# Kernel optimization log

Measured on AMD Instinct MI355X. Metric: run time of the kernel, lower is better.

Reference implementation:

```python
import jax, jax.numpy as jnp
import numpy as np

N = 64000      # total nodes in batched graph (16 graphs x 4000)
E = 1024000    # total edges (avg degree 16)
D = 512        # input/output feature dim
KTOT = 2048    # total assign dim (128 clusters per graph)
B = 16         # batch size (number of graphs)


def setup_inputs() -> dict:
    key = jax.random.key(0)
    ks = jax.random.split(key, 5)
    feat = jax.random.normal(ks[0], (N, D), jnp.float32)
    W_feat = jax.random.normal(ks[1], (D, D), jnp.float32) / np.float32(np.sqrt(D))
    b_feat = jnp.zeros((D,), jnp.float32)
    W_pool = jax.random.normal(ks[2], (D, KTOT), jnp.float32) / np.float32(np.sqrt(D))
    b_pool = jnp.zeros((KTOT,), jnp.float32)
    src = jax.random.randint(ks[3], (E,), 0, N, dtype=jnp.int32)
    dst = jax.random.randint(ks[4], (E,), 0, N, dtype=jnp.int32)
    return {"feat": feat, "W_feat": W_feat, "b_feat": b_feat,
            "W_pool": W_pool, "b_pool": b_pool,
            "src": src, "dst": dst, "batch_size": B}


def _gin(x, src, dst, W, b):
    """GIN layer with mean aggregator: relu(W @ (x + mean_neighbors(x)) + b)."""
    n = x.shape[0]
    agg = jax.ops.segment_sum(x[src], dst, num_segments=n)              # [N, d_in]
    deg = jax.ops.segment_sum(jnp.ones((src.shape[0],), x.dtype), dst, num_segments=n)
    agg = agg / jnp.maximum(deg, 1.0)[:, None]
    return jax.nn.relu((x + agg) @ W + b)


def reference(feat, W_feat, b_feat, W_pool, b_pool, src, dst, batch_size):
    n = feat.shape[0]
    ktot = W_pool.shape[1]
    n_per = n // batch_size      # equal-sized graphs (batch_num_nodes)
    k_per = ktot // batch_size   # clusters per graph

    h_feat = _gin(feat, src, dst, W_feat, b_feat)    # [N, D]
    assign = _gin(feat, src, dst, W_pool, b_pool)    # [N, KTOT]

    # block_diag mask: node of graph b may only assign to columns of graph b
    gid_node = jnp.arange(n) // n_per                # [N]
    gid_col = jnp.arange(ktot) // k_per              # [KTOT]
    mask = (gid_node[:, None] == gid_col[None, :]).astype(assign.dtype)

    # allennlp masked_softmax(memory_efficient=False):
    # softmax(x * mask) * mask, renormalized with +1e-13
    s = jax.nn.softmax(assign * mask, axis=-1) * mask
    s = s / (s.sum(axis=-1, keepdims=True) + 1e-13)  # [N, KTOT]

    h = s.T @ h_feat                                 # [KTOT, D]
    # sparse adj @ S via edge-list scatter: (A S)[i] = sum_{(i,j) in E} S[j]
    adj_s = jax.ops.segment_sum(s[dst], src, num_segments=n)  # [N, KTOT]
    adj_new = s.T @ adj_s                            # [KTOT, KTOT]
    return adj_new, h
```

## Files before the change

### kernel.cpp

```cpp
#include <hip/hip_runtime.h>
#include <math.h>

constexpr int N  = 64000;
constexpr int E  = 1024000;
constexpr int D  = 512;
constexpr int KT = 2048;
constexpr int B  = 16;
constexpr int NP = 4000;
constexpr int KP = 128;
constexpr int NR = N / 256;
constexpr int EPB = 2048;
constexpr int NPB = E / EPB;
constexpr int RSTRIDE = 4608;
constexpr int BSTRIDE = 4608;

typedef __attribute__((ext_vector_type(4))) float f32x4;
typedef __attribute__((ext_vector_type(2))) float f32x2;
typedef __attribute__((ext_vector_type(8))) short bf16x8;
typedef __attribute__((ext_vector_type(8))) unsigned short u16x8;

__device__ __forceinline__ unsigned short f2bf(float f) {
    unsigned u = __builtin_bit_cast(unsigned, f);
    return (unsigned short)((u + 0x7FFFu + ((u >> 16) & 1u)) >> 16);
}
__device__ __forceinline__ float bf2f(unsigned short h) {
    unsigned u = (unsigned)h << 16;
    return __builtin_bit_cast(float, u);
}

__device__ __forceinline__ unsigned char f2fp8_sw(float f) {
    unsigned u = __builtin_bit_cast(unsigned, f);
    unsigned s = u >> 31;
    float a = fabsf(f);
    if (a > 448.f) a = 448.f;
    unsigned code;
    if (a < 0.015625f) {
        code = (unsigned)rintf(a * 512.0f);
    } else {
        unsigned au = __builtin_bit_cast(unsigned, a);
        unsigned mant = au & 0x7FFFFFu;
        unsigned rnd = 0x7FFFFu + ((mant >> 20) & 1u);
        unsigned r2 = au + rnd;
        int e = (int)(r2 >> 23) - 127;
        unsigned m3 = (r2 >> 20) & 7u;
        if (e > 8) { e = 8; m3 = 7; }
        code = (unsigned)((e + 7) << 3) | m3;
    }
    return (unsigned char)(code | (s << 7));
}
__device__ __forceinline__ float fp82f_sw(unsigned b) {
    unsigned s = b >> 7, e = (b >> 3) & 15u, m = b & 7u;
    float vn = __builtin_bit_cast(float, ((e + 120u) << 23) | (m << 20));
    float vs = (float)(int)m * 0x1p-9f;
    float v = e ? vn : vs;
    return s ? -v : v;
}

__device__ __forceinline__ unsigned char f2fp8(float f) {
#if __has_builtin(__builtin_amdgcn_cvt_pk_fp8_f32)
    int w = __builtin_amdgcn_cvt_pk_fp8_f32(f, 0.f, 0, false);
    return (unsigned char)(w & 0xFF);
#else
    return f2fp8_sw(f);
#endif
}

__device__ __forceinline__ unsigned pack4_fp8(float f0, float f1, float f2, float f3) {
#if __has_builtin(__builtin_amdgcn_cvt_pk_fp8_f32)
    int w = __builtin_amdgcn_cvt_pk_fp8_f32(f0, f1, 0, false);
    w = __builtin_amdgcn_cvt_pk_fp8_f32(f2, f3, w, true);
    return (unsigned)w;
#else
    return (unsigned)f2fp8_sw(f0) | ((unsigned)f2fp8_sw(f1) << 8) |
           ((unsigned)f2fp8_sw(f2) << 16) | ((unsigned)f2fp8_sw(f3) << 24);
#endif
}

__device__ __forceinline__ void acc8_fp8(float* a, uint2 w) {
#if __has_builtin(__builtin_amdgcn_cvt_pk_f32_fp8)
    f32x2 p0 = __builtin_amdgcn_cvt_pk_f32_fp8((int)w.x, false);
    f32x2 p1 = __builtin_amdgcn_cvt_pk_f32_fp8((int)w.x, true);
    f32x2 p2 = __builtin_amdgcn_cvt_pk_f32_fp8((int)w.y, false);
    f32x2 p3 = __builtin_amdgcn_cvt_pk_f32_fp8((int)w.y, true);
    a[0] += p0.x; a[1] += p0.y; a[2] += p1.x; a[3] += p1.y;
    a[4] += p2.x; a[5] += p2.y; a[6] += p3.x; a[7] += p3.y;
#else
    #pragma unroll
    for (int q = 0; q < 4; ++q) a[q] += fp82f_sw((w.x >> (8 * q)) & 255u);
    #pragma unroll
    for (int q = 0; q < 4; ++q) a[4 + q] += fp82f_sw((w.y >> (8 * q)) & 255u);
#endif
}

typedef const __attribute__((address_space(1))) unsigned int* gas_u32p;
typedef __attribute__((address_space(3))) unsigned int* las_u32p;
__device__ __forceinline__ void glds16(const unsigned short* g, unsigned short* l) {
    __builtin_amdgcn_global_load_lds((gas_u32p)(const void*)g, (las_u32p)(void*)l, 16, 0, 0);
}

__device__ __forceinline__ int block_incl_scan(int v, int* ws) {
    int t = threadIdx.x, lane = t & 63, w = t >> 6;
    int x = v;
    #pragma unroll
    for (int off = 1; off < 64; off <<= 1) {
        int y = __shfl_up(x, off);
        if (lane >= off) x += y;
    }
    if (lane == 63) ws[w] = x;
    __syncthreads();
    if (t < 4) {
        int s = ws[t];
        #pragma unroll
        for (int off = 1; off < 4; off <<= 1) {
            int y = __shfl_up(s, off);
            if (t >= off) s += y;
        }
        ws[t] = s;
    }
    __syncthreads();
    return x + (w > 0 ? ws[w - 1] : 0);
}

__global__ __launch_bounds__(256) void k_cvt(const float* __restrict__ in,
                                             unsigned short* __restrict__ outb,
                                             unsigned char* __restrict__ out8,
                                             long long n) {
    long long i = ((long long)blockIdx.x * 256 + threadIdx.x) * 8;
    if (i >= n) return;
    f32x4 a = *(const f32x4*)&in[i];
    f32x4 b = *(const f32x4*)&in[i + 4];
    u16x8 o;
    o[0] = f2bf(a.x); o[1] = f2bf(a.y); o[2] = f2bf(a.z); o[3] = f2bf(a.w);
    o[4] = f2bf(b.x); o[5] = f2bf(b.y); o[6] = f2bf(b.z); o[7] = f2bf(b.w);
    *(u16x8*)&outb[i] = o;
    uint2 w;
    w.x = pack4_fp8(a.x, a.y, a.z, a.w);
    w.y = pack4_fp8(b.x, b.y, b.z, b.w);
    *(uint2*)&out8[i] = w;
}

__global__ void k_zrow(unsigned short* __restrict__ fb,
                       unsigned short* __restrict__ scb,
                       unsigned short* __restrict__ hfb,
                       unsigned char* __restrict__ f8b,
                       unsigned char* __restrict__ sc8) {
    int t = threadIdx.x;
    const u16x8 Z = {0, 0, 0, 0, 0, 0, 0, 0};
    if (t < 64)        *(u16x8*)&fb[(size_t)N * D + t * 8] = Z;
    else if (t < 80)   *(u16x8*)&scb[(size_t)N * KP + (t - 64) * 8] = Z;
    else if (t < 144)  *(u16x8*)&hfb[(size_t)N * D + (t - 80) * 8] = Z;
    else if (t < 176)  *(u16x8*)&f8b[(size_t)N * D + (size_t)(t - 144) * 16] = Z;
    else if (t < 184)  *(u16x8*)&sc8[(size_t)N * KP + (size_t)(t - 176) * 16] = Z;
}

__global__ __launch_bounds__(256) void k_transpose(const float* __restrict__ in,
                                                   unsigned short* __restrict__ out,
                                                   int R, int C) {
    __shared__ float tile[32][33];
    int bx = blockIdx.x * 32, by = blockIdx.y * 32;
    int tx = threadIdx.x & 31, ty = threadIdx.x >> 5;
    #pragma unroll
    for (int i = 0; i < 32; i += 8)
        if (by + ty + i < R && bx + tx < C)
            tile[ty + i][tx] = in[(size_t)(by + ty + i) * C + bx + tx];
    __syncthreads();
    #pragma unroll
    for (int i = 0; i < 32; i += 8)
        if (bx + ty + i < C && by + tx < R)
            out[(size_t)(bx + ty + i) * R + by + tx] = f2bf(tile[tx][ty + i]);
}

__global__ void k_init(int* __restrict__ rcur, int* __restrict__ bcur) {
    int t = threadIdx.x;
    if (t < NR) rcur[t] = t * RSTRIDE;
    bcur[t] = t * BSTRIDE;
}

__global__ __launch_bounds__(256) void k_split(const int* __restrict__ src,
                                               const int* __restrict__ dst,
                                               int* __restrict__ rcur, int2* __restrict__ out1,
                                               int* __restrict__ bcur, int2* __restrict__ out2) {
    __shared__ int2 stg[EPB];
    __shared__ int h[256], lstart[256], gbase[256];
    __shared__ int ws[4];
    int t = threadIdx.x;
    int e0 = blockIdx.x * EPB;
    int sv[8], dv[8], bin[8], rank[8];
    #pragma unroll
    for (int i = 0; i < 8; ++i) {
        int e = e0 + t + i * 256;
        sv[i] = src[e]; dv[i] = dst[e];
    }
    h[t] = 0;
    __syncthreads();
    #pragma unroll
    for (int i = 0; i < 8; ++i) {
        bin[i] = dv[i] >> 8;
        rank[i] = atomicAdd(&h[bin[i]], 1);
    }
    __syncthreads();
    {
        int v = h[t];
        int incl = block_incl_scan(v, ws);
        lstart[t] = incl - v;
        gbase[t] = v ? atomicAdd(&rcur[t], v) : 0;
    }
    __syncthreads();
    #pragma unroll
    for (int i = 0; i < 8; ++i)
        stg[lstart[bin[i]] + rank[i]] = int2{sv[i], dv[i]};
    __syncthreads();
    for (int i = t; i < EPB; i += 256) {
        int2 e = stg[i];
        int b = e.y >> 8;
        out1[gbase[b] + i - lstart[b]] = e;
    }
    __syncthreads();
    h[t] = 0;
    __syncthreads();
    #pragma unroll
    for (int i = 0; i < 8; ++i) {
        bin[i] = (sv[i] / NP) * B + dv[i] / NP;
        rank[i] = atomicAdd(&h[bin[i]], 1);
    }
    __syncthreads();
    {
        int v = h[t];
        int incl = block_incl_scan(v, ws);
        lstart[t] = incl - v;
        gbase[t] = v ? atomicAdd(&bcur[t], v) : 0;
    }
    __syncthreads();
    #pragma unroll
    for (int i = 0; i < 8; ++i)
        stg[lstart[bin[i]] + rank[i]] = int2{sv[i], dv[i]};
    __syncthreads();
    for (int i = t; i < EPB; i += 256) {
        int2 e = stg[i];
        int b = (e.x / NP) * B + e.y / NP;
        out2[gbase[b] + i - lstart[b]] = e;
    }
}

__global__ __launch_bounds__(256) void k_part2(const int2* __restrict__ pairs,
                                               const int* __restrict__ rcur,
                                               int* __restrict__ rowstart,
                                               int* __restrict__ degv,
                                               int* __restrict__ csr) {
    __shared__ int h[256];
    __shared__ int ws[4];
    int t = threadIdx.x;
    int r = blockIdx.x;
    int p0 = r * RSTRIDE, p1 = rcur[r];
    h[t] = 0;
    __syncthreads();
    for (int p = p0 + t; p < p1; p += 256)
        atomicAdd(&h[pairs[p].y & 255], 1);
    __syncthreads();
    int v = h[t];
    int incl = block_incl_scan(v, ws);
    int start = p0 + incl - v;
    __syncthreads();
    h[t] = start;
    rowstart[r * 256 + t] = start;
    degv[r * 256 + t] = v;
    __syncthreads();
    for (int p = p0 + t; p < p1; p += 256) {
        int2 e = pairs[p];
        int pos = atomicAdd(&h[e.y & 255], 1);
        csr[pos] = e.x;
    }
}

__global__ __launch_bounds__(256) void k_agg(const unsigned short* __restrict__ fb,
                                             const unsigned char* __restrict__ f8,
                                             const int* __restrict__ rowstart,
                                             const int* __restrict__ degv,
                                             const int* __restrict__ csr,
                                             unsigned short* __restrict__ xb) {
    int w = threadIdx.x >> 6, lane = threadIdx.x & 63;
    int node = blockIdx.x * 4 + w;
    int r0 = rowstart[node], dg = degv[node], r1 = r0 + dg;
    u16x8 self = *(const u16x8*)&fb[(size_t)node * D + lane * 8];
    float a[8] = {};
    for (int base = r0; base < r1; base += 64) {
        int ii = base + lane;
        int idx = N;
        if (ii < r1) idx = csr[ii];
        int cnt = r1 - base; if (cnt > 64) cnt = 64;
        int batches = (cnt + 7) & ~7;
        for (int j = 0; j < batches; j += 8) {
            int s0 = __shfl(idx, j + 0), s1 = __shfl(idx, j + 1);
            int s2 = __shfl(idx, j + 2), s3 = __shfl(idx, j + 3);
            int s4 = __shfl(idx, j + 4), s5 = __shfl(idx, j + 5);
            int s6 = __shfl(idx, j + 6), s7 = __shfl(idx, j + 7);
            uint2 g0 = *(const uint2*)&f8[(size_t)s0 * D + lane * 8];
            uint2 g1 = *(const uint2*)&f8[(size_t)s1 * D + lane * 8];
            uint2 g2 = *(const uint2*)&f8[(size_t)s2 * D + lane * 8];
            uint2 g3 = *(const uint2*)&f8[(size_t)s3 * D + lane * 8];
            uint2 g4 = *(const uint2*)&f8[(size_t)s4 * D + lane * 8];
            uint2 g5 = *(const uint2*)&f8[(size_t)s5 * D + lane * 8];
            uint2 g6 = *(const uint2*)&f8[(size_t)s6 * D + lane * 8];
            uint2 g7 = *(const uint2*)&f8[(size_t)s7 * D + lane * 8];
            acc8_fp8(a, g0); acc8_fp8(a, g1); acc8_fp8(a, g2); acc8_fp8(a, g3);
            acc8_fp8(a, g4); acc8_fp8(a, g5); acc8_fp8(a, g6); acc8_fp8(a, g7);
        }
    }
    float inv = 1.0f / fmaxf((float)dg, 1.0f);
    u16x8 o;
    #pragma unroll
    for (int q = 0; q < 8; ++q) o[q] = f2bf(bf2f(self[q]) + a[q] * inv);
    *(u16x8*)&xb[(size_t)node * D + lane * 8] = o;
}

__global__ __launch_bounds__(256) void k_gemm_feat(const unsigned short* __restrict__ Xb,
                                                   const unsigned short* __restrict__ Wt,
                                                   const float* __restrict__ bias,
                                                   unsigned short* __restrict__ Hf) {
    __shared__ unsigned short As[128 * 64];
    __shared__ unsigned short Bs[128 * 64];
    int t = threadIdx.x, wid = t >> 6, lane = t & 63;
    int wm = wid >> 1, wn = wid & 1;
    int row0 = blockIdx.x * 128, col0 = blockIdx.y * 128;
    int r8 = lane >> 3, ch = (lane & 7) ^ r8;
    f32x4 acc[4][4] = {};
    for (int k0 = 0; k0 < D; k0 += 64) {
        #pragma unroll
        for (int i = 0; i < 4; ++i) {
            int rr = wid * 32 + i * 8;
            glds16(Xb + (size_t)(row0 + rr + r8) * D + k0 + ch * 8, As + rr * 64);
            glds16(Wt + (size_t)(col0 + rr + r8) * D + k0 + ch * 8, Bs + rr * 64);
        }
        __syncthreads();
        #pragma unroll
        for (int ks = 0; ks < 2; ++ks) {
            bf16x8 af[4], bfr[4];
            #pragma unroll
            for (int f = 0; f < 4; ++f) {
                int ra = wm * 64 + f * 16 + (lane & 15);
                af[f] = *(const bf16x8*)&As[ra * 64 + (((ks * 4 + (lane >> 4)) ^ (ra & 7)) << 3)];
                int rb = wn * 64 + f * 16 + (lane & 15);
                bfr[f] = *(const bf16x8*)&Bs[rb * 64 + (((ks * 4 + (lane >> 4)) ^ (rb & 7)) << 3)];
            }
            #pragma unroll
            for (int m = 0; m < 4; ++m)
                #pragma unroll
                for (int n = 0; n < 4; ++n)
                    acc[m][n] = __builtin_amdgcn_mfma_f32_16x16x32_bf16(af[m], bfr[n], acc[m][n], 0, 0, 0);
        }
        __syncthreads();
    }
    float bv[4];
    #pragma unroll
    for (int n = 0; n < 4; ++n) bv[n] = bias[col0 + wn * 64 + n * 16 + (lane & 15)];
    #pragma unroll
    for (int m = 0; m < 4; ++m)
        #pragma unroll
        for (int r = 0; r < 4; ++r) {
            int row = row0 + wm * 64 + m * 16 + (lane >> 4) * 4 + r;
            #pragma unroll
            for (int n = 0; n < 4; ++n) {
                int col = col0 + wn * 64 + n * 16 + (lane & 15);
                float v = fmaxf(acc[m][n][r] + bv[n], 0.f);
                Hf[(size_t)row * D + col] = f2bf(v);
            }
        }
}

__global__ __launch_bounds__(256) void k_gemm_pool(const unsigned short* __restrict__ Xb,
                                                   const unsigned short* __restrict__ Wpt,
                                                   const float* __restrict__ bp,
                                                   unsigned short* __restrict__ sc,
                                                   unsigned char* __restrict__ sc8) {
    __shared__ unsigned short As[128 * 64];
    __shared__ unsigned short Bs[128 * 64];
    int t = threadIdx.x, wid = t >> 6, lane = t & 63;
    int bm = blockIdx.x;
    int g  = blockIdx.y;
    int row0 = g * NP + bm * 128;
    int nrows = NP - bm * 128; if (nrows > 128) nrows = 128;
    int col0 = g * KP;
    int r8 = lane >> 3, ch = (lane & 7) ^ r8;
    f32x4 acc[2][8] = {};
    for (int k0 = 0; k0 < D; k0 += 64) {
        #pragma unroll
        for (int i = 0; i < 4; ++i) {
            int rr = wid * 32 + i * 8;
            glds16(Xb + (size_t)(row0 + rr + r8) * D + k0 + ch * 8, As + rr * 64);
            glds16(Wpt + (size_t)(col0 + rr + r8) * D + k0 + ch * 8, Bs + rr * 64);
        }
        __syncthreads();
        #pragma unroll
        for (int ks = 0; ks < 2; ++ks) {
            bf16x8 af[2], bfr[8];
            #pragma unroll
            for (int m = 0; m < 2; ++m) {
                int ra = wid * 32 + m * 16 + (lane & 15);
                af[m] = *(const bf16x8*)&As[ra * 64 + (((ks * 4 + (lane >> 4)) ^ (ra & 7)) << 3)];
            }
            #pragma unroll
            for (int n = 0; n < 8; ++n) {
                int rb = n * 16 + (lane & 15);
                bfr[n] = *(const bf16x8*)&Bs[rb * 64 + (((ks * 4 + (lane >> 4)) ^ (rb & 7)) << 3)];
            }
            #pragma unroll
            for (int m = 0; m < 2; ++m)
                #pragma unroll
                for (int n = 0; n < 8; ++n)
                    acc[m][n] = __builtin_amdgcn_mfma_f32_16x16x32_bf16(af[m], bfr[n], acc[m][n], 0, 0, 0);
        }
        __syncthreads();
    }
    float bv[8];
    #pragma unroll
    for (int n = 0; n < 8; ++n) bv[n] = bp[col0 + n * 16 + (lane & 15)];
    #pragma unroll
    for (int m = 0; m < 2; ++m)
        #pragma unroll
        for (int r = 0; r < 4; ++r) {
            float v[8];
            #pragma unroll
            for (int n = 0; n < 8; ++n) v[n] = fmaxf(acc[m][n][r] + bv[n], 0.f);
            float mx = v[0];
            #pragma unroll
            for (int n = 1; n < 8; ++n) mx = fmaxf(mx, v[n]);
            #pragma unroll
            for (int off = 1; off < 16; off <<= 1) mx = fmaxf(mx, __shfl_xor(mx, off));
            float ssum = 0.f;
            #pragma unroll
            for (int n = 0; n < 8; ++n) { v[n] = __expf(v[n] - mx); ssum += v[n]; }
            #pragma unroll
            for (int off = 1; off < 16; off <<= 1) ssum += __shfl_xor(ssum, off);
            float inv = 1.0f / ssum;
            int rowl = wid * 32 + m * 16 + (lane >> 4) * 4 + r;
            if (rowl < nrows) {
                #pragma unroll
                for (int n = 0; n < 8; ++n) {
                    float sv = v[n] * inv;
                    int col = n * 16 + (lane & 15);
                    sc[(size_t)(row0 + rowl) * KP + col] = f2bf(sv);
                    sc8[(size_t)(row0 + rowl) * KP + col] = f2fp8(sv * 16.0f);
                }
            }
        }
}

constexpr int VBASE = 4128;
constexpr int VB8   = 4128;
constexpr int ADJ_SPLIT = 4;
constexpr int KZ_H = 16;

__device__ __forceinline__ void uv_write(unsigned short* arr, int c0, int es,
                                         const u16x8& l0, const u16x8& l1,
                                         const u16x8& l2, const u16x8& l3) {
    #pragma unroll
    for (int q = 0; q < 8; ++q) {
        int r0 = c0 + q, r1 = c0 + 8 + q, r2 = c0 + 16 + q, r3 = c0 + 24 + q;
        arr[r0 * 32 + (es ^ (((r0 >> 1) & 3) << 3))] = l0[q];
        arr[r1 * 32 + (es ^ (((r1 >> 1) & 3) << 3))] = l1[q];
        arr[r2 * 32 + (es ^ (((r2 >> 1) & 3) << 3))] = l2[q];
        arr[r3 * 32 + (es ^ (((r3 >> 1) & 3) << 3))] = l3[q];
    }
}

__device__ __forceinline__ void row_load(const unsigned short* row,
                                         u16x8& l0, u16x8& l1, u16x8& l2, u16x8& l3) {
    l0 = *(const u16x8*)(row);
    l1 = *(const u16x8*)(row + 8);
    l2 = *(const u16x8*)(row + 16);
    l3 = *(const u16x8*)(row + 24);
}

__device__ __forceinline__ bf16x8 uv_read(const unsigned short* UV, int base,
                                          int row, int chunk) {
    int c = chunk ^ ((row >> 1) & 3);
    return *(const bf16x8*)&UV[base + row * 32 + c * 8];
}

__device__ __forceinline__ void h_body(unsigned short* UV,
                                       const unsigned short* __restrict__ sc,
                                       const unsigned short* __restrict__ hf,
                                       float* __restrict__ outH,
                                       int g, int nt, int kz) {
    int t = threadIdx.x, wid = t >> 6, lane = t & 63;
    int n0 = nt * 128;
    int i0 = g * NP + kz * (NP / KZ_H), i1 = i0 + NP / KZ_H;
    int c0 = wid * 32;
    int es = lane & 31, op = lane >> 5;
    unsigned short* arr = &UV[op * VBASE];
    f32x4 acc[2][8] = {};

    const unsigned short* baseptr = op ? (hf + n0 + c0) : (sc + c0);
    int rstride = op ? D : KP;
    auto mkrow = [&](int tbase) -> const unsigned short* {
        int nd = tbase + es;
        nd = nd < i1 ? nd : N;
        return baseptr + (size_t)nd * rstride;
    };

    u16x8 a0, a1, a2, a3, b0, b1, b2, b3;
    row_load(mkrow(i0), a0, a1, a2, a3);
    row_load(mkrow(i0 + 32), b0, b1, b2, b3);

    int ntile = (i1 - i0 + 31) >> 5;
    for (int tt = 0; tt < ntile; tt += 2) {
        __syncthreads();
        uv_write(arr, c0, es, a0, a1, a2, a3);
        __syncthreads();
        row_load(mkrow(i0 + (tt + 2) * 32), a0, a1, a2, a3);
        {
            bf16x8 af[2], bfr[8];
            #pragma unroll
            for (int m = 0; m < 2; ++m)
                af[m] = uv_read(UV, 0, wid * 32 + m * 16 + (lane & 15), lane >> 4);
            #pragma unroll
            for (int n = 0; n < 8; ++n)
                bfr[n] = uv_read(UV, VBASE, n * 16 + (lane & 15), lane >> 4);
            #pragma unroll
            for (int m = 0; m < 2; ++m)
                #pragma unroll
                for (int n = 0; n < 8; ++n)
                    acc[m][n] = __builtin_amdgcn_mfma_f32_16x16x32_bf16(af[m], bfr[n], acc[m][n], 0, 0, 0);
        }
        __syncthreads();
        uv_write(arr, c0, es, b0, b1, b2, b3);
        __syncthreads();
        row_load(mkrow(i0 + (tt + 3) * 32), b0, b1, b2, b3);
        {
            bf16x8 af[2], bfr[8];
            #pragma unroll
            for (int m = 0; m < 2; ++m)
                af[m] = uv_read(UV, 0, wid * 32 + m * 16 + (lane & 15), lane >> 4);
            #pragma unroll
            for (int n = 0; n < 8; ++n)
                bfr[n] = uv_read(UV, VBASE, n * 16 + (lane & 15), lane >> 4);
            #pragma unroll
            for (int m = 0; m < 2; ++m)
                #pragma unroll
                for (int n = 0; n < 8; ++n)
                    acc[m][n] = __builtin_amdgcn_mfma_f32_16x16x32_bf16(af[m], bfr[n], acc[m][n], 0, 0, 0);
        }
    }
    #pragma unroll
    for (int m = 0; m < 2; ++m)
        #pragma unroll
        for (int r = 0; r < 4; ++r) {
            int row = g * KP + wid * 32 + m * 16 + (lane >> 4) * 4 + r;
            #pragma unroll
            for (int n = 0; n < 8; ++n) {
                int col = n0 + n * 16 + (lane & 15);
                atomicAdd(&outH[(size_t)row * D + col], acc[m][n][r]);
            }
        }
}

__device__ __forceinline__ void uv_write8(unsigned char* arr, int c0, int es,
                                          const uint4& lo, const uint4& hi) {
    const unsigned* wsrc = (const unsigned*)&lo;
    const unsigned* wsrc2 = (const unsigned*)&hi;
    int eb = es & 7, ec = es >> 3;
    #pragma unroll
    for (int q = 0; q < 8; ++q) {
        unsigned w0 = wsrc[q >> 1], w1 = wsrc2[q >> 1];
        #pragma unroll
        for (int hb = 0; hb < 2; ++hb) {
            int qi = q * 2 + hb;
            {
                int row = c0 + qi;
                unsigned byte = (wsrc[qi >> 2] >> ((qi & 3) * 8)) & 255u;
                arr[row * 32 + (((ec ^ ((row >> 2) & 3)) << 3) | eb)] = (unsigned char)byte;
            }
            {
                int row = c0 + 16 + qi;
                unsigned byte = (wsrc2[qi >> 2] >> ((qi & 3) * 8)) & 255u;
                arr[row * 32 + (((ec ^ ((row >> 2) & 3)) << 3) | eb)] = (unsigned char)byte;
            }
        }
    }
}

__device__ __forceinline__ long long uv_read8(const unsigned char* UV8, int base,
                                              int row, int chunk) {
    int c = chunk ^ ((row >> 2) & 3);
    return *(const long long*)&UV8[base + row * 32 + c * 8];
}

__device__ __forceinline__ void adj_body(unsigned char* UV8,
                                         const unsigned char* __restrict__ sc8,
                                         const int2* __restrict__ bpairs,
                                         const int* __restrict__ bcur,
                                         float* __restrict__ outA,
                                         int g1, int g2, int part) {
    int t = threadIdx.x, wid = t >> 6, lane = t & 63;
    int b = g1 * B + g2;
    int e0 = b * BSTRIDE, e1 = bcur[b], cnt = e1 - e0;
    int s0 = e0 + (int)((long long)cnt * part / ADJ_SPLIT);
    int s1 = e0 + (int)((long long)cnt * (part + 1) / ADJ_SPLIT);
    int c0 = wid * 32;
    int es = lane & 31, op = lane >> 5;
    unsigned char* arr = &UV8[op * VB8];
    f32x4 acc[2][8] = {};

    auto mkrow = [&](int tbase) -> const unsigned char* {
        int idx = tbase + es;
        bool v = idx < s1;
        int2 e = bpairs[v ? idx : s0];
        int node = v ? (op ? e.y : e.x) : N;
        return sc8 + (size_t)node * KP + c0;
    };

    uint4 alo, ahi, blo, bhi;
    { const unsigned char* r = mkrow(s0);      alo = *(const uint4*)r; ahi = *(const uint4*)(r + 16); }
    { const unsigned char* r = mkrow(s0 + 32); blo = *(const uint4*)r; bhi = *(const uint4*)(r + 16); }

    int ntile = (s1 - s0 + 31) >> 5;
    for (int tt = 0; tt < ntile; tt += 2) {
        __syncthreads();
        uv_write8(arr, c0, es, alo, ahi);
        __syncthreads();
        { const unsigned char* r = mkrow(s0 + (tt + 2) * 32); alo = *(const uint4*)r; ahi = *(const uint4*)(r + 16); }
        {
            long long af[2], bfr[8];
            #pragma unroll
            for (int m = 0; m < 2; ++m)
                af[m] = uv_read8(UV8, 0, wid * 32 + m * 16 + (lane & 15), lane >> 4);
            #pragma unroll
            for (int n = 0; n < 8; ++n)
                bfr[n] = uv_read8(UV8, VB8, n * 16 + (lane & 15), lane >> 4);
            #pragma unroll
            for (int m = 0; m < 2; ++m)
                #pragma unroll
                for (int n = 0; n < 8; ++n)
                    acc[m][n] = __builtin_amdgcn_mfma_f32_16x16x32_fp8_fp8(af[m], bfr[n], acc[m][n], 0, 0, 0);
        }
        __syncthreads();
        uv_write8(arr, c0, es, blo, bhi);
        __syncthreads();
        { const unsigned char* r = mkrow(s0 + (tt + 3) * 32); blo = *(const uint4*)r; bhi = *(const uint4*)(r + 16); }
        {
            long long af[2], bfr[8];
            #pragma unroll
            for (int m = 0; m < 2; ++m)
                af[m] = uv_read8(UV8, 0, wid * 32 + m * 16 + (lane & 15), lane >> 4);
            #pragma unroll
            for (int n = 0; n < 8; ++n)
                bfr[n] = uv_read8(UV8, VB8, n * 16 + (lane & 15), lane >> 4);
            #pragma unroll
            for (int m = 0; m < 2; ++m)
                #pragma unroll
                for (int n = 0; n < 8; ++n)
                    acc[m][n] = __builtin_amdgcn_mfma_f32_16x16x32_fp8_fp8(af[m], bfr[n], acc[m][n], 0, 0, 0);
        }
    }
    const float DS = 1.0f / 256.0f;
    #pragma unroll
    for (int m = 0; m < 2; ++m)
        #pragma unroll
        for (int r = 0; r < 4; ++r) {
            int row = g1 * KP + wid * 32 + m * 16 + (lane >> 4) * 4 + r;
            #pragma unroll
            for (int n = 0; n < 8; ++n) {
                int col = g2 * KP + n * 16 + (lane & 15);
                atomicAdd(&outA[(size_t)row * KT + col], acc[m][n][r] * DS);
            }
        }
}

__global__ __launch_bounds__(256) void k_ha(const unsigned short* __restrict__ sc,
                                            const unsigned char* __restrict__ sc8,
                                            const unsigned short* __restrict__ hf,
                                            const int2* __restrict__ bpairs,
                                            const int* __restrict__ bcur,
                                            float* __restrict__ outH,
                                            float* __restrict__ outA) {
    __shared__ __align__(16) unsigned short UV[8224];
    int lin = blockIdx.x;
    int role = (lin >> 8) & 1;
    int base = (lin >> 9) * 256 + (lin & 255);
    if (role == 0) {
        int xcd = base & 7, idx = base >> 3;
        int g1 = 2 * xcd + (idx & 1);
        int g2 = (idx >> 1) & 15;
        int part = (idx >> 5) & 3;
        adj_body((unsigned char*)UV, sc8, bpairs, bcur, outA, g1, g2, part);
    } else {
        int g = base & 15, nt = (base >> 4) & 3, kz = base >> 6;
        h_body(UV, sc, hf, outH, g, nt, kz);
    }
}

extern "C" void kernel_launch(void* const* d_in, const int* in_sizes, int n_in,
                              void* d_out, int out_size, void* d_ws, size_t ws_size,
                              hipStream_t stream) {
    const float* feat   = (const float*)d_in[0];
    const float* W_feat = (const float*)d_in[1];
    const float* b_feat = (const float*)d_in[2];
    const float* W_pool = (const float*)d_in[3];
    const float* b_pool = (const float*)d_in[4];
    const int*   src    = (const int*)d_in[5];
    const int*   dst    = (const int*)d_in[6];

    char* w = (char*)d_ws;
    unsigned short* fb  = (unsigned short*)w; w += (size_t)(N + 1) * D * 2;
    unsigned char*  f8b = (unsigned char*)w;  w += (size_t)(N + 1) * D;
    unsigned short* xb  = (unsigned short*)w; w += (size_t)N * D * 2;
    unsigned short* hfb = (unsigned short*)w; w += (size_t)(N + 1) * D * 2;
    unsigned short* scb = (unsigned short*)w; w += (size_t)(N + 1) * KP * 2;
    unsigned char*  sc8 = (unsigned char*)w;  w += (size_t)(N + 1) * KP;
    unsigned short* Wt  = (unsigned short*)w; w += (size_t)D * D * 2;
    unsigned short* Wpt = (unsigned short*)w; w += (size_t)KT * D * 2;
    int2* pairs1  = (int2*)w; w += (size_t)NR * RSTRIDE * 8;
    int2* bpairs  = (int2*)w; w += (size_t)256 * BSTRIDE * 8;
    int*  csr     = (int*)w;  w += ((size_t)NR * RSTRIDE + 64) * 4;
    int*  rowstart= (int*)w;  w += (size_t)N * 4;
    int*  degv    = (int*)w;  w += (size_t)N * 4;
    int*  rcur    = (int*)w;  w += NR * 4;
    int*  bcur    = (int*)w;  w += 256 * 4;

    hipMemsetAsync(d_out, 0, (size_t)out_size * sizeof(float), stream);

    k_cvt<<<(int)(((long long)N * D) / (8 * 256)), 256, 0, stream>>>(feat, fb, f8b, (long long)N * D);
    k_zrow<<<1, 256, 0, stream>>>(fb, scb, hfb, f8b, sc8);
    dim3 gt1(D / 32, D / 32);
    k_transpose<<<gt1, 256, 0, stream>>>(W_feat, Wt, D, D);
    dim3 gt2(KT / 32, D / 32);
    k_transpose<<<gt2, 256, 0, stream>>>(W_pool, Wpt, D, KT);

    k_init<<<1, 256, 0, stream>>>(rcur, bcur);
    k_split<<<NPB, 256, 0, stream>>>(src, dst, rcur, pairs1, bcur, bpairs);
    k_part2<<<NR, 256, 0, stream>>>(pairs1, rcur, rowstart, degv, csr);

    k_agg<<<N / 4, 256, 0, stream>>>(fb, f8b, rowstart, degv, csr, xb);
    dim3 gf(N / 128, D / 128);
    k_gemm_feat<<<gf, 256, 0, stream>>>(xb, Wt, b_feat, hfb);
    dim3 gp(32, B);
    k_gemm_pool<<<gp, 256, 0, stream>>>(xb, Wpt, b_pool, scb, sc8);

    k_ha<<<2048, 256, 0, stream>>>(scb, sc8, hfb, bpairs, bcur,
                                   (float*)d_out + (size_t)KT * KT, (float*)d_out);
}
```

Before: 407.8 us.

## Split edge bucketing into two passes and double adjacency work split

```diff
diff --git a/kernel.cpp b/kernel.cpp
--- a/kernel.cpp
+++ b/kernel.cpp
@@ -176,10 +176,9 @@
     bcur[t] = t * BSTRIDE;
 }
 
-__global__ __launch_bounds__(256) void k_split(const int* __restrict__ src,
-                                               const int* __restrict__ dst,
-                                               int* __restrict__ rcur, int2* __restrict__ out1,
-                                               int* __restrict__ bcur, int2* __restrict__ out2) {
+__global__ __launch_bounds__(256) void k_splitA(const int* __restrict__ src,
+                                                const int* __restrict__ dst,
+                                                int* __restrict__ rcur, int2* __restrict__ out1) {
     __shared__ int2 stg[EPB];
     __shared__ int h[256], lstart[256], gbase[256];
     __shared__ int ws[4];
@@ -215,13 +214,32 @@
         int b = e.y >> 8;
         out1[gbase[b] + i - lstart[b]] = e;
     }
-    __syncthreads();
+}
+
+__global__ __launch_bounds__(256) void k_splitB(const int2* __restrict__ pairs,
+                                                const int* __restrict__ rcur,
+                                                int* __restrict__ bcur, int2* __restrict__ out2) {
+    __shared__ int2 stg[RSTRIDE / 2];
+    __shared__ int h[256], lstart[256], gbase[256];
+    __shared__ int ws[4];
+    int t = threadIdx.x;
+    int r = blockIdx.x >> 1, half = blockIdx.x & 1;
+    int p0 = r * RSTRIDE, p1 = rcur[r], len = p1 - p0;
+    int s0 = p0 + (len * half) / 2;
+    int s1 = p0 + (len * (half + 1)) / 2;
+    int cnt = s1 - s0;
+    int sv[9], dv[9], bin[9], rank[9];
     h[t] = 0;
     __syncthreads();
     #pragma unroll
-    for (int i = 0; i < 8; ++i) {
-        bin[i] = (sv[i] / NP) * B + dv[i] / NP;
-        rank[i] = atomicAdd(&h[bin[i]], 1);
+    for (int i = 0; i < 9; ++i) {
+        int p = s0 + t + i * 256;
+        if (p < s1) {
+            int2 e = pairs[p];
+            sv[i] = e.x; dv[i] = e.y;
+            bin[i] = (e.x / NP) * B + e.y / NP;
+            rank[i] = atomicAdd(&h[bin[i]], 1);
+        }
     }
     __syncthreads();
     {
@@ -232,10 +250,13 @@
     }
     __syncthreads();
     #pragma unroll
-    for (int i = 0; i < 8; ++i)
-        stg[lstart[bin[i]] + rank[i]] = int2{sv[i], dv[i]};
-    __syncthreads();
-    for (int i = t; i < EPB; i += 256) {
+    for (int i = 0; i < 9; ++i) {
+        int p = s0 + t + i * 256;
+        if (p < s1)
+            stg[lstart[bin[i]] + rank[i]] = int2{sv[i], dv[i]};
+    }
+    __syncthreads();
+    for (int i = t; i < cnt; i += 256) {
         int2 e = stg[i];
         int b = (e.x / NP) * B + e.y / NP;
         out2[gbase[b] + i - lstart[b]] = e;
@@ -447,7 +468,7 @@
 
 constexpr int VBASE = 4128;
 constexpr int VB8   = 4128;
-constexpr int ADJ_SPLIT = 4;
+constexpr int ADJ_SPLIT = 8;
 constexpr int KZ_H = 16;
 
 __device__ __forceinline__ void uv_write(unsigned short* arr, int c0, int es,
@@ -560,21 +581,16 @@
     const unsigned* wsrc2 = (const unsigned*)&hi;
     int eb = es & 7, ec = es >> 3;
     #pragma unroll
-    for (int q = 0; q < 8; ++q) {
-        unsigned w0 = wsrc[q >> 1], w1 = wsrc2[q >> 1];
-        #pragma unroll
-        for (int hb = 0; hb < 2; ++hb) {
-            int qi = q * 2 + hb;
-            {
-                int row = c0 + qi;
-                unsigned byte = (wsrc[qi >> 2] >> ((qi & 3) * 8)) & 255u;
-                arr[row * 32 + (((ec ^ ((row >> 2) & 3)) << 3) | eb)] = (unsigned char)byte;
-            }
-            {
-                int row = c0 + 16 + qi;
-                unsigned byte = (wsrc2[qi >> 2] >> ((qi & 3) * 8)) & 255u;
-                arr[row * 32 + (((ec ^ ((row >> 2) & 3)) << 3) | eb)] = (unsigned char)byte;
-            }
+    for (int qi = 0; qi < 16; ++qi) {
+        {
+            int row = c0 + qi;
+            unsigned byte = (wsrc[qi >> 2] >> ((qi & 3) * 8)) & 255u;
+            arr[row * 32 + (((ec ^ ((row >> 2) & 3)) << 3) | eb)] = (unsigned char)byte;
+        }
+        {
+            int row = c0 + 16 + qi;
+            unsigned byte = (wsrc2[qi >> 2] >> ((qi & 3) * 8)) & 255u;
+            arr[row * 32 + (((ec ^ ((row >> 2) & 3)) << 3) | eb)] = (unsigned char)byte;
         }
     }
 }
@@ -675,17 +691,19 @@
                                             float* __restrict__ outA) {
     __shared__ __align__(16) unsigned short UV[8224];
     int lin = blockIdx.x;
-    int role = (lin >> 8) & 1;
-    int base = (lin >> 9) * 256 + (lin & 255);
-    if (role == 0) {
+    int k = lin >> 8, rem = lin & 255;
+    if (k % 3 == 2) {
+        int hbase = (k / 3) * 256 + rem;
+        int g = hbase & 15, nt = (hbase >> 4) & 3, kz = hbase >> 6;
+        h_body(UV, sc, hf, outH, g, nt, kz);
+    } else {
+        int adjIdx = k - (k + 1) / 3;
+        int base = adjIdx * 256 + rem;
         int xcd = base & 7, idx = base >> 3;
         int g1 = 2 * xcd + (idx & 1);
         int g2 = (idx >> 1) & 15;
-        int part = (idx >> 5) & 3;
+        int part = (idx >> 5) & 7;
         adj_body((unsigned char*)UV, sc8, bpairs, bcur, outA, g1, g2, part);
-    } else {
-        int g = base & 15, nt = (base >> 4) & 3, kz = base >> 6;
-        h_body(UV, sc, hf, outH, g, nt, kz);
     }
 }
 
@@ -727,7 +745,8 @@
     k_transpose<<<gt2, 256, 0, stream>>>(W_pool, Wpt, D, KT);
 
     k_init<<<1, 256, 0, stream>>>(rcur, bcur);
-    k_split<<<NPB, 256, 0, stream>>>(src, dst, rcur, pairs1, bcur, bpairs);
+    k_splitA<<<NPB, 256, 0, stream>>>(src, dst, rcur, pairs1);
+    k_splitB<<<2 * NR, 256, 0, stream>>>(pairs1, rcur, bcur, bpairs);
     k_part2<<<NR, 256, 0, stream>>>(pairs1, rcur, rowstart, degv, csr);
 
     k_agg<<<N / 4, 256, 0, stream>>>(fb, f8b, rowstart, degv, csr, xb);
@@ -736,6 +755,6 @@
     dim3 gp(32, B);
     k_gemm_pool<<<gp, 256, 0, stream>>>(xb, Wpt, b_pool, scb, sc8);
 
-    k_ha<<<2048, 256, 0, stream>>>(scb, sc8, hfb, bpairs, bcur,
+    k_ha<<<3072, 256, 0, stream>>>(scb, sc8, hfb, bpairs, bcur,
                                    (float*)d_out + (size_t)KT * KT, (float*)d_out);
 }
```

After: 448.3 us. +9.9%, slower.
